# Kernel optimization log

Hardware: AMD Instinct MI355X
Metric: run time of the kernel (lower is better)

Reference implementation:

```python
import jax, jax.numpy as jnp
import numpy as np

K = 3  # kernel_size


def _build_grid(offset, H, W):
    """Vectorized version of the original double for-loop grid build.

    Original: for x in range(W), y in range(H):
        anchor = ([x, y] - [W-1, H-1]/2) / ([W-1, H-1]/2)
        fgrid[:, K*y:K*y+K, K*x:K*x+K, :] = offset[:, :, x, y].view(B, K, K, 2) + anchor
    Note offset is indexed [:, :, x, y] (x over range(W) on the H axis) -- requires H == W.
    """
    B = offset.shape[0]
    assert H == W, "original indexing offset[:, :, x, y] assumes square maps"
    o = offset.reshape(B, K, K, 2, H, W)          # [B, j, i, c, x-axis, y-axis]
    # -> [B, y, j, x, i, c] so rows are K*y+j, cols are K*x+i
    o = jnp.transpose(o, (0, 5, 1, 4, 2, 3))
    half_w = (W - 1) / 2.0
    half_h = (H - 1) / 2.0
    ax = ((jnp.arange(W, dtype=offset.dtype) - half_w) / half_w)  # anchor x-coord, indexed by x
    ay = ((jnp.arange(H, dtype=offset.dtype) - half_h) / half_h)  # anchor y-coord, indexed by y
    anch = jnp.stack(jnp.broadcast_arrays(ax[None, :], ay[:, None]), axis=-1)  # [H(y), W(x), 2]
    grid = o + anch[None, :, None, :, None, :]
    return grid.reshape(B, H * K, W * K, 2)


def _grid_sample_bilinear(img, grid):
    """F.grid_sample(img, grid, mode='bilinear', padding_mode='zeros', align_corners=False)."""
    B, C, H, W = img.shape
    gx, gy = grid[..., 0], grid[..., 1]          # [B, Ho, Wo]
    ix = ((gx + 1.0) * W - 1.0) * 0.5            # unnormalize, align_corners=False
    iy = ((gy + 1.0) * H - 1.0) * 0.5
    ix0 = jnp.floor(ix)
    iy0 = jnp.floor(iy)
    wx1 = ix - ix0
    wy1 = iy - iy0
    flat = img.reshape(B, C, H * W)

    def gather(xi, yi):
        valid = ((xi >= 0) & (xi <= W - 1) & (yi >= 0) & (yi <= H - 1))
        xc = jnp.clip(xi, 0, W - 1).astype(jnp.int32)
        yc = jnp.clip(yi, 0, H - 1).astype(jnp.int32)
        lin = (yc * W + xc).reshape(B, -1)       # [B, Ho*Wo]
        g = jax.vmap(lambda f, l: f[:, l])(flat, lin)  # [B, C, Ho*Wo]
        g = g.reshape(B, C, *xi.shape[1:])
        return g * valid[:, None].astype(img.dtype)

    out = (gather(ix0, iy0) * ((1 - wx1) * (1 - wy1))[:, None]
           + gather(ix0 + 1, iy0) * (wx1 * (1 - wy1))[:, None]
           + gather(ix0, iy0 + 1) * ((1 - wx1) * wy1)[:, None]
           + gather(ix0 + 1, iy0 + 1) * (wx1 * wy1)[:, None])
    return out


def setup_inputs() -> dict:
    key = jax.random.key(0)
    k1, k2, k3 = jax.random.split(key, 3)
    B, C, H, W = 32, 128, 56, 56
    OUTC = 256
    feature = jax.random.normal(k1, (B, C, H, W), dtype=jnp.float32)
    offset = jax.random.normal(k2, (B, 2 * K * K, H, W), dtype=jnp.float32) * 0.1
    conv_weight = jax.random.normal(k3, (OUTC, C, K, K), dtype=jnp.float32) * 0.05
    return {"feature": feature, "offset": offset, "conv_weight": conv_weight}


def reference(feature, offset, conv_weight):
    B, C, H, W = feature.shape
    grid = _build_grid(offset, H, W)                      # [B, H*K, W*K, 2]
    deformed = _grid_sample_bilinear(feature, grid)       # [B, C, H*K, W*K]
    out = jax.lax.conv_general_dilated(
        deformed, conv_weight, window_strides=(K, K), padding="VALID",
        dimension_numbers=("NCHW", "OIHW", "NCHW"))      # [B, OUTC, H, W]
    return out
```

## Files before the change

kernel.cpp:

```cpp
#include <hip/hip_runtime.h>
#include <hip/hip_bf16.h>
#include <stdint.h>

#define KTAPS 9
#define C_IN 128
#define C_OUT 256
#define HW 56
#define PLANE 3136
#define BATCH 32
#define NPX (BATCH * PLANE)
#define KTOT 1152
#define PXB 64
#define NBLK (NPX / PXB)
#define BLK_PER_XCD (NBLK / 8)

typedef __attribute__((ext_vector_type(8))) _Float16 f16x8;
typedef __attribute__((ext_vector_type(4))) float f32x4;

static __device__ __forceinline__ uint16_t f2h(float f) {
    _Float16 h = (_Float16)f;
    uint16_t u;
    __builtin_memcpy(&u, &h, 2);
    return u;
}

__global__ void k_feat_nhwc(const float* __restrict__ f, unsigned short* __restrict__ fws) {
    __shared__ float tile[C_IN * 57];
    int blk = blockIdx.x;
    int b = blk / HW, y = blk % HW;
    const float* src = f + (size_t)b * C_IN * PLANE + y * HW;
    for (int i = threadIdx.x; i < C_IN * HW; i += 256) {
        int c = i / HW, x = i % HW;
        tile[c * 57 + x] = src[(size_t)c * PLANE + x];
    }
    __syncthreads();
    unsigned short* dst = fws + (size_t)blk * HW * C_IN;
    for (int j = threadIdx.x; j < HW * C_IN; j += 256) {
        int x = j >> 7, c = j & 127;
        dst[j] = f2h(tile[c * 57 + x]);
    }
}

__global__ void k_weight(const float* __restrict__ w, unsigned short* __restrict__ W2) {
    int idx = blockIdx.x * 256 + threadIdx.x;
    if (idx >= C_OUT * KTOT) return;
    int oc = idx / KTOT, r = idx % KTOT;
    int t = r >> 7, ic = r & 127;
    int j = t / 3, i = t % 3;
    W2[idx] = f2h(w[((oc * C_IN + ic) * 3 + j) * 3 + i]);
}

__global__ void k_coords(const float* __restrict__ off, float* __restrict__ sxy) {
    __shared__ float tile[HW * 57];
    int blk = blockIdx.x;
    int b = blk / 18, tc = blk % 18;
    const float* src = off + (size_t)blk * PLANE;
    for (int i = threadIdx.x; i < PLANE; i += 256) {
        int xx = i / HW, yy = i % HW;
        tile[xx * 57 + yy] = src[i];
    }
    __syncthreads();
    float* dst = sxy + (size_t)tc * NPX + (size_t)b * PLANE;
    bool isx = (tc & 1) == 0;
    for (int p = threadIdx.x; p < PLANE; p += 256) {
        int y = p / HW, x = p % HW;
        float v = tile[x * 57 + y];
        float a = isx ? ((float)x - 27.5f) * (1.0f / 27.5f)
                      : ((float)y - 27.5f) * (1.0f / 27.5f);
        dst[p] = (v + a + 1.0f) * 28.0f - 0.5f;
    }
}

__global__ __launch_bounds__(256, 3) void k_main(const unsigned short* __restrict__ fws,
                                                 const unsigned short* __restrict__ W2,
                                                 const float* __restrict__ sxy,
                                                 float* __restrict__ out) {
    __shared__ __align__(16) unsigned char Vs[2][PXB * 256];
    __shared__ float cs[18][PXB];
    const int tid = threadIdx.x;
    const int wave = tid >> 6, lane = tid & 63;
    const int l16 = lane & 15, grp = lane >> 4;
    const int bid = blockIdx.x;
    const int lbid = (bid & 7) * BLK_PER_XCD + (bid >> 3);
    const int px0 = lbid * PXB;
    const int fb_s = (px0 / PLANE) * (PLANE * C_IN);

    for (int i = tid; i < 18 * PXB; i += 256) {
        int tc = i >> 6, p = i & (PXB - 1);
        cs[tc][p] = sxy[(size_t)tc * NPX + px0 + p];
    }
    __syncthreads();

    f32x4 acc[4][4];
#pragma unroll
    for (int m = 0; m < 4; m++)
#pragma unroll
        for (int n = 0; n < 4; n++) acc[m][n] = (f32x4)0.0f;

    f16x8 sv[4];
    float sw[4];
    f16x8 A[2][4];

    auto issue1 = [&](int t, int r) {
        int p = wave * 16 + r * 4 + grp;
        float ixv = cs[2 * t][p];
        float iyv = cs[2 * t + 1][p];
        const unsigned short* fb = fws + fb_s;
        float fx0 = floorf(ixv), fy0 = floorf(iyv);
        float wx1 = ixv - fx0, wy1 = iyv - fy0;
        float wx0 = 1.0f - wx1, wy0 = 1.0f - wy1;
        int ix0 = (int)fx0, iy0 = (int)fy0;
        int ix1 = ix0 + 1, iy1 = iy0 + 1;
        float vx0 = ((unsigned)ix0 < HW) ? 1.0f : 0.0f;
        float vx1 = ((unsigned)ix1 < HW) ? 1.0f : 0.0f;
        float vy0 = ((unsigned)iy0 < HW) ? 1.0f : 0.0f;
        float vy1 = ((unsigned)iy1 < HW) ? 1.0f : 0.0f;
        int xc0 = min(max(ix0, 0), HW - 1), xc1 = min(max(ix1, 0), HW - 1);
        int yc0 = min(max(iy0, 0), HW - 1), yc1 = min(max(iy1, 0), HW - 1);
        const unsigned short* r0 = fb + (size_t)(yc0 * HW) * C_IN + l16 * 8;
        const unsigned short* r1 = fb + (size_t)(yc1 * HW) * C_IN + l16 * 8;
        sv[0] = *(const f16x8*)(r0 + xc0 * C_IN);
        sv[1] = *(const f16x8*)(r0 + xc1 * C_IN);
        sv[2] = *(const f16x8*)(r1 + xc0 * C_IN);
        sv[3] = *(const f16x8*)(r1 + xc1 * C_IN);
        sw[0] = wx0 * wy0 * vx0 * vy0;
        sw[1] = wx1 * wy0 * vx1 * vy0;
        sw[2] = wx0 * wy1 * vx0 * vy1;
        sw[3] = wx1 * wy1 * vx1 * vy1;
    };

    auto finish1 = [&](int buf, int r) {
        int p = wave * 16 + r * 4 + grp;
        f16x8 v = sv[0] * (f16x8)(_Float16)sw[0]
                + sv[1] * (f16x8)(_Float16)sw[1]
                + sv[2] * (f16x8)(_Float16)sw[2]
                + sv[3] * (f16x8)(_Float16)sw[3];
        int byteoff = p * 256 + ((l16 * 16) ^ ((p & 7) << 4));
        *(f16x8*)(&Vs[buf][byteoff]) = v;
    };

    auto loadA = [&](int slot, int t, int ks) {
        const unsigned short* wb = W2 + (size_t)(wave * 64 + l16) * KTOT + t * 128 + ks * 32 + grp * 8;
#pragma unroll
        for (int mt = 0; mt < 4; mt++)
            A[slot][mt] = *(const f16x8*)(wb + (size_t)(mt * 16) * KTOT);
    };

    auto gemm_ks = [&](int ks, int buf, int slot) {
        f16x8 bv[4];
#pragma unroll
        for (int nt = 0; nt < 4; nt++) {
            int pxl = nt * 16 + l16;
            int kbyte = ks * 64 + grp * 16;
            bv[nt] = *(const f16x8*)(&Vs[buf][pxl * 256 + (kbyte ^ ((pxl & 7) << 4))]);
        }
#pragma unroll
        for (int mt = 0; mt < 4; mt++)
#pragma unroll
            for (int nt = 0; nt < 4; nt++)
                acc[mt][nt] = __builtin_amdgcn_mfma_f32_16x16x32_f16(A[slot][mt], bv[nt], acc[mt][nt], 0, 0, 0);
    };

    loadA(0, 0, 0);
#pragma unroll
    for (int r = 0; r < 4; r++) {
        issue1(0, r);
        finish1(0, r);
    }
    __syncthreads();

    for (int t = 0; t < KTAPS; t++) {
        const int buf = t & 1, nbuf = buf ^ 1;
        const bool more = (t < KTAPS - 1);
        loadA(1, t, 1);
        if (more) issue1(t + 1, 0);
        gemm_ks(0, buf, 0);
        if (more) finish1(nbuf, 0);
        loadA(0, t, 2);
        if (more) issue1(t + 1, 1);
        gemm_ks(1, buf, 1);
        if (more) finish1(nbuf, 1);
        loadA(1, t, 3);
        if (more) issue1(t + 1, 2);
        gemm_ks(2, buf, 0);
        if (more) finish1(nbuf, 2);
        if (more) loadA(0, t + 1, 0);
        if (more) issue1(t + 1, 3);
        gemm_ks(3, buf, 1);
        if (more) finish1(nbuf, 3);
        __syncthreads();
    }

#pragma unroll
    for (int nt = 0; nt < 4; nt++) {
        int pp0 = px0 + nt * 16;
        int bb = pp0 / PLANE;
        int rr = pp0 - bb * PLANE;
        float* ob = out + (size_t)bb * C_OUT * PLANE + rr + l16;
#pragma unroll
        for (int mt = 0; mt < 4; mt++) {
#pragma unroll
            for (int r = 0; r < 4; r++) {
                int oc = wave * 64 + mt * 16 + grp * 4 + r;
                ob[(size_t)oc * PLANE] = acc[mt][nt][r];
            }
        }
    }
}

extern "C" void kernel_launch(void* const* d_in, const int* in_sizes, int n_in,
                              void* d_out, int out_size, void* d_ws, size_t ws_size,
                              hipStream_t stream) {
    const float* feature = (const float*)d_in[0];
    const float* offset = (const float*)d_in[1];
    const float* weight = (const float*)d_in[2];
    float* out = (float*)d_out;

    char* ws = (char*)d_ws;
    unsigned short* fws = (unsigned short*)ws;
    unsigned short* W2 = (unsigned short*)(ws + 25690112);
    float* sxy = (float*)(ws + 25690112 + 589824);

    k_feat_nhwc<<<BATCH * HW, 256, 0, stream>>>(feature, fws);
    k_weight<<<(C_OUT * KTOT + 255) / 256, 256, 0, stream>>>(weight, W2);
    k_coords<<<BATCH * 18, 256, 0, stream>>>(offset, sxy);
    k_main<<<NBLK, 256, 0, stream>>>(fws, W2, sxy, out);
}
```

Baseline: 202.4 us.

## Pre-swizzle weights into MFMA fragment order and peel last tap iteration

The weight-prep kernel now writes fp16 weights in the exact per-wave, per-lane fragment order the MFMA loop consumes. Each A-fragment load becomes a contiguous, fully coalesced 16-byte-per-lane read instead of a strided row gather, and it is issued as a nontemporal load. The tap loop is made branch-free and kept rolled, with the final tap peeled out, so the per-iteration `more` predicates disappear. The risks are that nontemporal hints may hurt cache reuse of weights shared by all blocks, and that keeping the loop rolled may change scheduling.

```diff
diff --git a/kernel.cpp b/kernel.cpp
--- a/kernel.cpp
+++ b/kernel.cpp
@@ -41,13 +41,22 @@
     }
 }
 
-__global__ void k_weight(const float* __restrict__ w, unsigned short* __restrict__ W2) {
+__global__ void k_weight(const float* __restrict__ w, unsigned short* __restrict__ W3) {
     int idx = blockIdx.x * 256 + threadIdx.x;
     if (idx >= C_OUT * KTOT) return;
-    int oc = idx / KTOT, r = idx % KTOT;
-    int t = r >> 7, ic = r & 127;
+    int e = idx & 7;
+    int r1 = idx >> 3;
+    int lane = r1 & 63;
+    int r2 = r1 >> 6;
+    int mt = r2 & 3;
+    int r3 = r2 >> 2;
+    int wave = r3 & 3;
+    int bk = r3 >> 2;
+    int t = bk >> 2, ks = bk & 3;
+    int oc = wave * 64 + mt * 16 + (lane & 15);
+    int ic = ks * 32 + (lane >> 4) * 8 + e;
     int j = t / 3, i = t % 3;
-    W2[idx] = f2h(w[((oc * C_IN + ic) * 3 + j) * 3 + i]);
+    W3[idx] = f2h(w[((oc * C_IN + ic) * 3 + j) * 3 + i]);
 }
 
 __global__ void k_coords(const float* __restrict__ off, float* __restrict__ sxy) {
@@ -72,7 +81,7 @@
 }
 
 __global__ __launch_bounds__(256, 3) void k_main(const unsigned short* __restrict__ fws,
-                                                 const unsigned short* __restrict__ W2,
+                                                 const unsigned short* __restrict__ W3,
                                                  const float* __restrict__ sxy,
                                                  float* __restrict__ out) {
     __shared__ __align__(16) unsigned char Vs[2][PXB * 256];
@@ -140,10 +149,10 @@
     };
 
     auto loadA = [&](int slot, int t, int ks) {
-        const unsigned short* wb = W2 + (size_t)(wave * 64 + l16) * KTOT + t * 128 + ks * 32 + grp * 8;
+        const unsigned short* wb = W3 + ((size_t)(((t * 4 + ks) * 4 + wave) * 4) * 64 + lane) * 8;
 #pragma unroll
         for (int mt = 0; mt < 4; mt++)
-            A[slot][mt] = *(const f16x8*)(wb + (size_t)(mt * 16) * KTOT);
+            A[slot][mt] = __builtin_nontemporal_load((const f16x8*)(wb + mt * 512));
     };
 
     auto gemm_ks = [&](int ks, int buf, int slot) {
@@ -169,27 +178,35 @@
     }
     __syncthreads();
 
-    for (int t = 0; t < KTAPS; t++) {
+#pragma unroll 1
+    for (int t = 0; t < KTAPS - 1; t++) {
         const int buf = t & 1, nbuf = buf ^ 1;
-        const bool more = (t < KTAPS - 1);
         loadA(1, t, 1);
-        if (more) issue1(t + 1, 0);
+        issue1(t + 1, 0);
         gemm_ks(0, buf, 0);
-        if (more) finish1(nbuf, 0);
+        finish1(nbuf, 0);
         loadA(0, t, 2);
-        if (more) issue1(t + 1, 1);
+        issue1(t + 1, 1);
         gemm_ks(1, buf, 1);
-        if (more) finish1(nbuf, 1);
+        finish1(nbuf, 1);
         loadA(1, t, 3);
-        if (more) issue1(t + 1, 2);
+        issue1(t + 1, 2);
         gemm_ks(2, buf, 0);
-        if (more) finish1(nbuf, 2);
-        if (more) loadA(0, t + 1, 0);
-        if (more) issue1(t + 1, 3);
+        finish1(nbuf, 2);
+        loadA(0, t + 1, 0);
+        issue1(t + 1, 3);
         gemm_ks(3, buf, 1);
-        if (more) finish1(nbuf, 3);
+        finish1(nbuf, 3);
         __syncthreads();
     }
+
+    loadA(1, 8, 1);
+    gemm_ks(0, 0, 0);
+    loadA(0, 8, 2);
+    gemm_ks(1, 0, 1);
+    loadA(1, 8, 3);
+    gemm_ks(2, 0, 0);
+    gemm_ks(3, 0, 1);
 
 #pragma unroll
     for (int nt = 0; nt < 4; nt++) {
@@ -218,11 +235,11 @@
 
     char* ws = (char*)d_ws;
     unsigned short* fws = (unsigned short*)ws;
-    unsigned short* W2 = (unsigned short*)(ws + 25690112);
+    unsigned short* W3 = (unsigned short*)(ws + 25690112);
     float* sxy = (float*)(ws + 25690112 + 589824);
 
     k_feat_nhwc<<<BATCH * HW, 256, 0, stream>>>(feature, fws);
-    k_weight<<<(C_OUT * KTOT + 255) / 256, 256, 0, stream>>>(weight, W2);
+    k_weight<<<(C_OUT * KTOT + 255) / 256, 256, 0, stream>>>(weight, W3);
     k_coords<<<BATCH * 18, 256, 0, stream>>>(offset, sxy);
-    k_main<<<NBLK, 256, 0, stream>>>(fws, W2, sxy, out);
-}
+    k_main<<<NBLK, 256, 0, stream>>>(fws, W3, sxy, out);
+}
```

Result: slower. 245.9 us (+21.5%).

## Have each wave own 16 pixels across all output channels, drop LDS staging

Applied to the files above, without the earlier changes.

The main kernel is reorganized so each wave samples its own 16 pixels directly into registers and computes all 256 output channels for them. This removes the shared-memory sample buffer, its swizzled stores and loads, and the per-tap block barriers. The weights are pre-permuted into an MFMA-fragment-ordered layout so each lane reads contiguous 16-byte chunks. In exchange every wave now reads the full weight slice per k-step (16 fragments) from global memory or cache, the wave holds 64 accumulator registers, and the occupancy hint is lowered from 3 to 2 blocks.

```diff
diff --git a/kernel.cpp b/kernel.cpp
--- a/kernel.cpp
+++ b/kernel.cpp
@@ -41,13 +41,18 @@
     }
 }
 
-__global__ void k_weight(const float* __restrict__ w, unsigned short* __restrict__ W2) {
+__global__ void k_weight(const float* __restrict__ w, unsigned short* __restrict__ W3) {
     int idx = blockIdx.x * 256 + threadIdx.x;
     if (idx >= C_OUT * KTOT) return;
-    int oc = idx / KTOT, r = idx % KTOT;
-    int t = r >> 7, ic = r & 127;
+    int e = idx & 7;
+    int lane = (idx >> 3) & 63;
+    int mtg = (idx >> 9) & 15;
+    int ks = (idx >> 13) & 3;
+    int t = idx >> 15;
+    int oc = mtg * 16 + (lane & 15);
+    int ic = ks * 32 + (lane >> 4) * 8 + e;
     int j = t / 3, i = t % 3;
-    W2[idx] = f2h(w[((oc * C_IN + ic) * 3 + j) * 3 + i]);
+    W3[idx] = f2h(w[((oc * C_IN + ic) * 3 + j) * 3 + i]);
 }
 
 __global__ void k_coords(const float* __restrict__ off, float* __restrict__ sxy) {
@@ -71,11 +76,10 @@
     }
 }
 
-__global__ __launch_bounds__(256, 3) void k_main(const unsigned short* __restrict__ fws,
-                                                 const unsigned short* __restrict__ W2,
+__global__ __launch_bounds__(256, 2) void k_main(const unsigned short* __restrict__ fws,
+                                                 const unsigned short* __restrict__ W3,
                                                  const float* __restrict__ sxy,
                                                  float* __restrict__ out) {
-    __shared__ __align__(16) unsigned char Vs[2][PXB * 256];
     __shared__ float cs[18][PXB];
     const int tid = threadIdx.x;
     const int wave = tid >> 6, lane = tid & 63;
@@ -83,29 +87,27 @@
     const int bid = blockIdx.x;
     const int lbid = (bid & 7) * BLK_PER_XCD + (bid >> 3);
     const int px0 = lbid * PXB;
-    const int fb_s = (px0 / PLANE) * (PLANE * C_IN);
+    const unsigned short* fb = fws + (size_t)(px0 / PLANE) * (PLANE * C_IN) + grp * 8;
 
     for (int i = tid; i < 18 * PXB; i += 256) {
-        int tc = i >> 6, p = i & (PXB - 1);
-        cs[tc][p] = sxy[(size_t)tc * NPX + px0 + p];
+        int tc = i >> 6, pp = i & (PXB - 1);
+        cs[tc][pp] = sxy[(size_t)tc * NPX + px0 + pp];
     }
     __syncthreads();
 
-    f32x4 acc[4][4];
-#pragma unroll
-    for (int m = 0; m < 4; m++)
-#pragma unroll
-        for (int n = 0; n < 4; n++) acc[m][n] = (f32x4)0.0f;
-
-    f16x8 sv[4];
-    float sw[4];
-    f16x8 A[2][4];
-
-    auto issue1 = [&](int t, int r) {
-        int p = wave * 16 + r * 4 + grp;
+    const int p = wave * 16 + l16;
+
+    f32x4 acc[16];
+#pragma unroll
+    for (int m = 0; m < 16; m++) acc[m] = (f32x4)0.0f;
+
+    f16x8 cv[4][4];
+    float swc[4], swn[4];
+    const unsigned short *c00, *c10, *c01, *c11;
+
+    auto calc_tap = [&](int t, float* sw) {
         float ixv = cs[2 * t][p];
         float iyv = cs[2 * t + 1][p];
-        const unsigned short* fb = fws + fb_s;
         float fx0 = floorf(ixv), fy0 = floorf(iyv);
         float wx1 = ixv - fx0, wy1 = iyv - fy0;
         float wx0 = 1.0f - wx1, wy0 = 1.0f - wy1;
@@ -117,92 +119,63 @@
         float vy1 = ((unsigned)iy1 < HW) ? 1.0f : 0.0f;
         int xc0 = min(max(ix0, 0), HW - 1), xc1 = min(max(ix1, 0), HW - 1);
         int yc0 = min(max(iy0, 0), HW - 1), yc1 = min(max(iy1, 0), HW - 1);
-        const unsigned short* r0 = fb + (size_t)(yc0 * HW) * C_IN + l16 * 8;
-        const unsigned short* r1 = fb + (size_t)(yc1 * HW) * C_IN + l16 * 8;
-        sv[0] = *(const f16x8*)(r0 + xc0 * C_IN);
-        sv[1] = *(const f16x8*)(r0 + xc1 * C_IN);
-        sv[2] = *(const f16x8*)(r1 + xc0 * C_IN);
-        sv[3] = *(const f16x8*)(r1 + xc1 * C_IN);
+        const unsigned short* r0 = fb + (size_t)(yc0 * HW) * C_IN;
+        const unsigned short* r1 = fb + (size_t)(yc1 * HW) * C_IN;
+        c00 = r0 + xc0 * C_IN; c10 = r0 + xc1 * C_IN;
+        c01 = r1 + xc0 * C_IN; c11 = r1 + xc1 * C_IN;
         sw[0] = wx0 * wy0 * vx0 * vy0;
         sw[1] = wx1 * wy0 * vx1 * vy0;
         sw[2] = wx0 * wy1 * vx0 * vy1;
         sw[3] = wx1 * wy1 * vx1 * vy1;
     };
 
-    auto finish1 = [&](int buf, int r) {
-        int p = wave * 16 + r * 4 + grp;
-        f16x8 v = sv[0] * (f16x8)(_Float16)sw[0]
-                + sv[1] * (f16x8)(_Float16)sw[1]
-                + sv[2] * (f16x8)(_Float16)sw[2]
-                + sv[3] * (f16x8)(_Float16)sw[3];
-        int byteoff = p * 256 + ((l16 * 16) ^ ((p & 7) << 4));
-        *(f16x8*)(&Vs[buf][byteoff]) = v;
+    auto sample_ks = [&](int ks) {
+        cv[0][ks] = *(const f16x8*)(c00 + ks * 32);
+        cv[1][ks] = *(const f16x8*)(c10 + ks * 32);
+        cv[2][ks] = *(const f16x8*)(c01 + ks * 32);
+        cv[3][ks] = *(const f16x8*)(c11 + ks * 32);
     };
 
-    auto loadA = [&](int slot, int t, int ks) {
-        const unsigned short* wb = W2 + (size_t)(wave * 64 + l16) * KTOT + t * 128 + ks * 32 + grp * 8;
-#pragma unroll
-        for (int mt = 0; mt < 4; mt++)
-            A[slot][mt] = *(const f16x8*)(wb + (size_t)(mt * 16) * KTOT);
-    };
-
-    auto gemm_ks = [&](int ks, int buf, int slot) {
-        f16x8 bv[4];
-#pragma unroll
-        for (int nt = 0; nt < 4; nt++) {
-            int pxl = nt * 16 + l16;
-            int kbyte = ks * 64 + grp * 16;
-            bv[nt] = *(const f16x8*)(&Vs[buf][pxl * 256 + (kbyte ^ ((pxl & 7) << 4))]);
+    calc_tap(0, swc);
+#pragma unroll
+    for (int ks = 0; ks < 4; ks++) sample_ks(ks);
+
+#pragma unroll
+    for (int t = 0; t < KTAPS; t++) {
+        const bool more = (t < KTAPS - 1);
+        if (more) calc_tap(t + 1, swn);
+#pragma unroll
+        for (int ks = 0; ks < 4; ks++) {
+            f16x8 v = cv[0][ks] * (f16x8)(_Float16)swc[0]
+                    + cv[1][ks] * (f16x8)(_Float16)swc[1]
+                    + cv[2][ks] * (f16x8)(_Float16)swc[2]
+                    + cv[3][ks] * (f16x8)(_Float16)swc[3];
+            const unsigned short* wb = W3 + (size_t)(t * 4 + ks) * 8192 + lane * 8;
+            f16x8 af[16];
+#pragma unroll
+            for (int mtg = 0; mtg < 16; mtg++)
+                af[mtg] = *(const f16x8*)(wb + mtg * 512);
+            if (more) sample_ks(ks);
+#pragma unroll
+            for (int mtg = 0; mtg < 16; mtg++)
+                acc[mtg] = __builtin_amdgcn_mfma_f32_16x16x32_f16(af[mtg], v, acc[mtg], 0, 0, 0);
         }
-#pragma unroll
-        for (int mt = 0; mt < 4; mt++)
-#pragma unroll
-            for (int nt = 0; nt < 4; nt++)
-                acc[mt][nt] = __builtin_amdgcn_mfma_f32_16x16x32_f16(A[slot][mt], bv[nt], acc[mt][nt], 0, 0, 0);
-    };
-
-    loadA(0, 0, 0);
-#pragma unroll
-    for (int r = 0; r < 4; r++) {
-        issue1(0, r);
-        finish1(0, r);
-    }
-    __syncthreads();
-
-    for (int t = 0; t < KTAPS; t++) {
-        const int buf = t & 1, nbuf = buf ^ 1;
-        const bool more = (t < KTAPS - 1);
-        loadA(1, t, 1);
-        if (more) issue1(t + 1, 0);
-        gemm_ks(0, buf, 0);
-        if (more) finish1(nbuf, 0);
-        loadA(0, t, 2);
-        if (more) issue1(t + 1, 1);
-        gemm_ks(1, buf, 1);
-        if (more) finish1(nbuf, 1);
-        loadA(1, t, 3);
-        if (more) issue1(t + 1, 2);
-        gemm_ks(2, buf, 0);
-        if (more) finish1(nbuf, 2);
-        if (more) loadA(0, t + 1, 0);
-        if (more) issue1(t + 1, 3);
-        gemm_ks(3, buf, 1);
-        if (more) finish1(nbuf, 3);
-        __syncthreads();
-    }
-
-#pragma unroll
-    for (int nt = 0; nt < 4; nt++) {
-        int pp0 = px0 + nt * 16;
-        int bb = pp0 / PLANE;
-        int rr = pp0 - bb * PLANE;
-        float* ob = out + (size_t)bb * C_OUT * PLANE + rr + l16;
-#pragma unroll
-        for (int mt = 0; mt < 4; mt++) {
+        if (more) {
+#pragma unroll
+            for (int c = 0; c < 4; c++) swc[c] = swn[c];
+        }
+    }
+
+    {
+        int bb = px0 / PLANE;
+        int rr = px0 - bb * PLANE + p;
+        float* ob = out + (size_t)bb * C_OUT * PLANE + rr;
+#pragma unroll
+        for (int mtg = 0; mtg < 16; mtg++) {
 #pragma unroll
             for (int r = 0; r < 4; r++) {
-                int oc = wave * 64 + mt * 16 + grp * 4 + r;
-                ob[(size_t)oc * PLANE] = acc[mt][nt][r];
+                int oc = mtg * 16 + grp * 4 + r;
+                ob[(size_t)oc * PLANE] = acc[mtg][r];
             }
         }
     }
@@ -218,11 +191,11 @@
 
     char* ws = (char*)d_ws;
     unsigned short* fws = (unsigned short*)ws;
-    unsigned short* W2 = (unsigned short*)(ws + 25690112);
+    unsigned short* W3 = (unsigned short*)(ws + 25690112);
     float* sxy = (float*)(ws + 25690112 + 589824);
 
     k_feat_nhwc<<<BATCH * HW, 256, 0, stream>>>(feature, fws);
-    k_weight<<<(C_OUT * KTOT + 255) / 256, 256, 0, stream>>>(weight, W2);
+    k_weight<<<(C_OUT * KTOT + 255) / 256, 256, 0, stream>>>(weight, W3);
     k_coords<<<BATCH * 18, 256, 0, stream>>>(offset, sxy);
-    k_main<<<NBLK, 256, 0, stream>>>(fws, W2, sxy, out);
-}
+    k_main<<<NBLK, 256, 0, stream>>>(fws, W3, sxy, out);
+}
```

New measurement: 260.1 us. 28.5% more time.
